# Kernel optimization log

Measured on AMD Instinct MI355X. Metric: run time of the kernel, lower is better.

## Reference

```python
import jax, jax.numpy as jnp
import numpy as np

B, C, K, D = 16, 128, 128, 256
EPS = 1e-5  # torch BatchNorm1d default eps


def _bn(x, gamma, beta):
    # torch BatchNorm1d training-mode on (N, ch, L): normalize each channel over (N, L)
    mean = x.mean(axis=(0, 2), keepdims=True)
    var = x.var(axis=(0, 2), keepdims=True)  # biased, matches torch normalization
    return (x - mean) / jnp.sqrt(var + EPS) * gamma[None, :, None] + beta[None, :, None]


def setup_inputs() -> dict:
    key = jax.random.key(0)
    ks = jax.random.split(key, 6)
    q = jax.random.normal(ks[0], (B, C, D), jnp.float32)
    kc = jax.random.normal(ks[1], (B, K, D), jnp.float32)
    W0 = jax.random.normal(ks[2], (D, D), jnp.float32) / np.sqrt(D)
    W1 = jax.random.normal(ks[3], (D, D), jnp.float32) / np.sqrt(D)
    cmask = jax.random.randint(ks[4], (B, C), 0, 2, jnp.int32)
    kmask = jax.random.randint(ks[5], (B, K), 0, 2, jnp.int32)
    klen = jnp.maximum(kmask.sum(axis=1), 1).astype(jnp.int32)
    return {
        "query_candidates_repr": q,
        "key_candidates": kc,
        "W0": W0,
        "W1": W1,
        "bn0_gamma": jnp.ones((C,), jnp.float32),
        "bn0_beta": jnp.zeros((C,), jnp.float32),
        "bn1_gamma": jnp.ones((K,), jnp.float32),
        "bn1_beta": jnp.zeros((K,), jnp.float32),
        "query_candidate_mask": cmask,
        "key_candidate_mask": kmask,
        "key_candidate_len": klen,
    }


def reference(query_candidates_repr, key_candidates, W0, W1,
              bn0_gamma, bn0_beta, bn1_gamma, bn1_beta,
              query_candidate_mask, key_candidate_mask, key_candidate_len):
    # gated_attention branch (att_type != 'softmax'), activate = tanh
    g0 = _bn(query_candidates_repr @ W0.T, bn0_gamma, bn0_beta)  # (B,C,D)
    g1 = _bn(key_candidates @ W1.T, bn1_gamma, bn1_beta)          # (B,K,D)
    # (B,C,K,D) gate product
    attention_weight = jax.nn.sigmoid(g1)[:, None, :, :] * jax.nn.sigmoid(g0)[:, :, None, :]
    attention_res = key_candidates[:, None, :, :] * attention_weight  # (B,C,K,D)
    mask = (query_candidate_mask[:, :, None] * key_candidate_mask[:, None, :]).astype(jnp.float32)
    attention_res_masked = attention_res * mask[..., None]
    attention_vector = attention_res_masked.sum(axis=2) / key_candidate_len[:, None, None].astype(jnp.float32)
    output_res = jnp.tanh(attention_vector)  # (B,C,D)
    return output_res, attention_res_masked, attention_weight.mean(axis=-1)
```

## Files before the change

kernel.cpp:

```cpp
#include <hip/hip_runtime.h>


#define NB 16
#define NC 128
#define NK 128
#define ND 256

__global__ __launch_bounds__(256) void k_gemm(const float* __restrict__ q,
                                              const float* __restrict__ kc,
                                              const float* __restrict__ W0,
                                              const float* __restrict__ W1,
                                              float* __restrict__ Y,
                                              float* __restrict__ tvec) {
    if (blockIdx.x == 0 && blockIdx.y == 0) {
        for (int i = threadIdx.x; i < NB * ND; i += 256) tvec[i] = 0.f;
    }
    __shared__ float As[16][64];
    __shared__ float Bs[16][64];
    const int m0 = blockIdx.x * 64;
    const int d0 = blockIdx.y * 64;
    const int t  = threadIdx.x;
    const float* A = (m0 < 2048) ? (q + (size_t)m0 * ND) : (kc + (size_t)(m0 - 2048) * ND);
    const float* W = (m0 < 2048) ? W0 : W1;
    const int ml = t >> 2;
    const int jl = (t & 3) * 4;
    const int ty = t >> 4;
    const int tx = t & 15;

    float acc[4][4] = {};
    for (int j0 = 0; j0 < 256; j0 += 16) {
        float4 a = *(const float4*)(A + ml * ND + j0 + jl);
        float4 b = *(const float4*)(W + (d0 + ml) * ND + j0 + jl);
        As[jl + 0][ml] = a.x; As[jl + 1][ml] = a.y; As[jl + 2][ml] = a.z; As[jl + 3][ml] = a.w;
        Bs[jl + 0][ml] = b.x; Bs[jl + 1][ml] = b.y; Bs[jl + 2][ml] = b.z; Bs[jl + 3][ml] = b.w;
        __syncthreads();
#pragma unroll
        for (int jj = 0; jj < 16; ++jj) {
            float4 av = *(const float4*)&As[jj][ty * 4];
            float4 bv = *(const float4*)&Bs[jj][tx * 4];
            acc[0][0] += av.x * bv.x; acc[0][1] += av.x * bv.y; acc[0][2] += av.x * bv.z; acc[0][3] += av.x * bv.w;
            acc[1][0] += av.y * bv.x; acc[1][1] += av.y * bv.y; acc[1][2] += av.y * bv.z; acc[1][3] += av.y * bv.w;
            acc[2][0] += av.z * bv.x; acc[2][1] += av.z * bv.y; acc[2][2] += av.z * bv.z; acc[2][3] += av.z * bv.w;
            acc[3][0] += av.w * bv.x; acc[3][1] += av.w * bv.y; acc[3][2] += av.w * bv.z; acc[3][3] += av.w * bv.w;
        }
        __syncthreads();
    }
#pragma unroll
    for (int i = 0; i < 4; ++i) {
        float4 o = make_float4(acc[i][0], acc[i][1], acc[i][2], acc[i][3]);
        *(float4*)(Y + (size_t)(m0 + ty * 4 + i) * ND + d0 + tx * 4) = o;
    }
}

__global__ __launch_bounds__(256) void k_sau(float* __restrict__ Y,
                                             const float* __restrict__ kc,
                                             const float* __restrict__ g0, const float* __restrict__ b0,
                                             const float* __restrict__ g1, const float* __restrict__ b1,
                                             const int* __restrict__ kmask,
                                             float* __restrict__ tvec) {
    const int ch = blockIdx.x;
    const int t  = threadIdx.x;
    const int rbase = (ch < 128) ? ch : (2048 + (ch - 128));
    float v[NB];
    float s = 0.f, s2 = 0.f;
#pragma unroll
    for (int b = 0; b < NB; ++b) {
        v[b] = Y[(size_t)(rbase + b * 128) * ND + t];
        s += v[b]; s2 += v[b] * v[b];
    }
#pragma unroll
    for (int off = 32; off > 0; off >>= 1) {
        s  += __shfl_down(s,  off, 64);
        s2 += __shfl_down(s2, off, 64);
    }
    __shared__ float r1[4], r2[4];
    __shared__ float bsc, bsh;
    const int w = t >> 6;
    if ((t & 63) == 0) { r1[w] = s; r2[w] = s2; }
    __syncthreads();
    if (t == 0) {
        s  = r1[0] + r1[1] + r1[2] + r1[3];
        s2 = r2[0] + r2[1] + r2[2] + r2[3];
        float mean = s * (1.f / 4096.f);
        float var  = s2 * (1.f / 4096.f) - mean * mean;
        float rstd = rsqrtf(var + 1e-5f);
        float g  = (ch < 128) ? g0[ch] : g1[ch - 128];
        float be = (ch < 128) ? b0[ch] : b1[ch - 128];
        bsc = g * rstd;
        bsh = be - mean * g * rstd;
    }
    __syncthreads();
    const float sc = bsc, sh = bsh;
    if (ch < 128) {
#pragma unroll
        for (int b = 0; b < NB; ++b) {
            float sig = 1.f / (1.f + __expf(-(v[b] * sc + sh)));
            Y[(size_t)(rbase + b * 128) * ND + t] = sig;
        }
    } else {
        const int k = ch - 128;
#pragma unroll
        for (int b = 0; b < NB; ++b) {
            float sig = 1.f / (1.f + __expf(-(v[b] * sc + sh)));
            Y[(size_t)(rbase + b * 128) * ND + t] = sig;
            if (kmask[b * 128 + k] != 0) {
                float u = kc[(size_t)(b * 128 + k) * ND + t] * sig;
                atomicAdd(&tvec[b * ND + t], u);
            }
        }
    }
}

__global__ __launch_bounds__(256) void k_tail(const float* __restrict__ Y,
                                              const float* __restrict__ kc,
                                              const int* __restrict__ cmask,
                                              const int* __restrict__ kmask,
                                              const int* __restrict__ klen,
                                              const float* __restrict__ tvec,
                                              float* __restrict__ out0,
                                              float* __restrict__ out1,
                                              float* __restrict__ out2) {
    __shared__ float As[16][64];
    __shared__ float Bs[16][64];
    const int bid = blockIdx.x;
    const int t   = threadIdx.x;

    if (bid < 64) {
        const int b  = bid >> 2;
        const int c0 = ((bid >> 1) & 1) * 64;
        const int k0 = (bid & 1) * 64;
        const float* A = Y + (size_t)(b * 128 + c0) * ND;
        const float* W = Y + (size_t)(2048 + b * 128 + k0) * ND;
        const int ml = t >> 2;
        const int jl = (t & 3) * 4;
        const int ty = t >> 4;
        const int tx = t & 15;
        float acc[4][4] = {};
        for (int j0 = 0; j0 < 256; j0 += 16) {
            float4 a  = *(const float4*)(A + ml * ND + j0 + jl);
            float4 bb = *(const float4*)(W + ml * ND + j0 + jl);
            As[jl + 0][ml] = a.x;  As[jl + 1][ml] = a.y;  As[jl + 2][ml] = a.z;  As[jl + 3][ml] = a.w;
            Bs[jl + 0][ml] = bb.x; Bs[jl + 1][ml] = bb.y; Bs[jl + 2][ml] = bb.z; Bs[jl + 3][ml] = bb.w;
            __syncthreads();
#pragma unroll
            for (int jj = 0; jj < 16; ++jj) {
                float4 av = *(const float4*)&As[jj][ty * 4];
                float4 bv = *(const float4*)&Bs[jj][tx * 4];
                acc[0][0] += av.x * bv.x; acc[0][1] += av.x * bv.y; acc[0][2] += av.x * bv.z; acc[0][3] += av.x * bv.w;
                acc[1][0] += av.y * bv.x; acc[1][1] += av.y * bv.y; acc[1][2] += av.y * bv.z; acc[1][3] += av.y * bv.w;
                acc[2][0] += av.z * bv.x; acc[2][1] += av.z * bv.y; acc[2][2] += av.z * bv.z; acc[2][3] += av.z * bv.w;
                acc[3][0] += av.w * bv.x; acc[3][1] += av.w * bv.y; acc[3][2] += av.w * bv.z; acc[3][3] += av.w * bv.w;
            }
            __syncthreads();
        }
        const float scale = 1.f / 256.f;
#pragma unroll
        for (int i = 0; i < 4; ++i) {
            float4 o = make_float4(acc[i][0] * scale, acc[i][1] * scale, acc[i][2] * scale, acc[i][3] * scale);
            *(float4*)(out2 + ((size_t)(b * 128 + c0 + ty * 4 + i)) * 128 + k0 + tx * 4) = o;
        }
    } else if (bid < 320) {
        const int local = bid - 64;
        const int b  = local >> 4;
        const int c0 = (local & 15) * 8;
        const float tv  = tvec[b * ND + t];
        const float inv = 1.f / (float)klen[b];
#pragma unroll
        for (int ci = 0; ci < 8; ++ci) {
            const int bc = b * 128 + c0 + ci;
            const float cm = (cmask[bc] != 0) ? 1.f : 0.f;
            const float s0 = Y[(size_t)bc * ND + t];
            out0[(size_t)bc * ND + t] = tanhf(cm * s0 * tv * inv);
        }
    } else {
        const int bc = bid - 320;
        const int b  = bc >> 7;
        const int f  = t & 63;
        const int g  = t >> 6;
        float4 s0v = *(const float4*)(Y + (size_t)bc * ND + f * 4);
        const bool cm = cmask[bc] != 0;
        float4 v0 = cm ? s0v : make_float4(0.f, 0.f, 0.f, 0.f);

        const float* s1p = Y  + (size_t)(2048 + b * 128 + g) * ND + f * 4;
        const float* kcp = kc + (size_t)(b * 128 + g) * ND + f * 4;
        const int*   kmb = kmask + b * 128;
        float*       op  = out1 + (size_t)bc * 128 * ND + (size_t)g * ND + f * 4;

#pragma unroll 4
        for (int k0 = 0; k0 < 32; ++k0) {
            const int k = k0 * 4 + g;
            const float km = (float)kmb[k];
            float4 s1v = *(const float4*)s1p;
            float4 kcv = *(const float4*)kcp;
            float4 o = make_float4(v0.x * km * kcv.x * s1v.x,
                                   v0.y * km * kcv.y * s1v.y,
                                   v0.z * km * kcv.z * s1v.z,
                                   v0.w * km * kcv.w * s1v.w);
            *(float4*)op = o;
            s1p += 4 * ND; kcp += 4 * ND; op += 4 * ND;
        }
    }
}

extern "C" void kernel_launch(void* const* d_in, const int* in_sizes, int n_in,
                              void* d_out, int out_size, void* d_ws, size_t ws_size,
                              hipStream_t stream) {
    const float* q     = (const float*)d_in[0];
    const float* kc    = (const float*)d_in[1];
    const float* W0    = (const float*)d_in[2];
    const float* W1    = (const float*)d_in[3];
    const float* g0    = (const float*)d_in[4];
    const float* b0    = (const float*)d_in[5];
    const float* g1    = (const float*)d_in[6];
    const float* b1    = (const float*)d_in[7];
    const int*   cmask = (const int*)d_in[8];
    const int*   kmask = (const int*)d_in[9];
    const int*   klen  = (const int*)d_in[10];

    float* ws = (float*)d_ws;
    float* Y  = ws;
    float* tv = ws + 1048576;

    float* o    = (float*)d_out;
    float* out0 = o;
    float* out1 = o + 524288;
    float* out2 = o + 67633152;

    k_gemm<<<dim3(64, 4), 256, 0, stream>>>(q, kc, W0, W1, Y, tv);
    k_sau <<<256,         256, 0, stream>>>(Y, kc, g0, b0, g1, b1, kmask, tv);
    k_tail<<<2368,        256, 0, stream>>>(Y, kc, cmask, kmask, klen, tv, out0, out1, out2);
}
```

Measured before the change: 324.4 us.

## Precompute masked key*gate product, remap blocks per XCD, use nontemporal stores

k_sau now writes a precomputed per-key product U = kmask*kc*sigmoid(g1) into the workspace. The big out1 write loop therefore reads one stream instead of two plus the mask. The block-to-(b,c) mapping is permuted so that consecutive block ids, which are spread across XCDs, share the same batch's U rows in each XCD's L2. Output stores for the 256MB out1 tensor become nontemporal to avoid polluting cache. This adds an extra 2MB write in k_sau in exchange.

```diff
diff --git a/kernel.cpp b/kernel.cpp
--- a/kernel.cpp
+++ b/kernel.cpp
@@ -5,6 +5,8 @@
 #define NC 128
 #define NK 128
 #define ND 256
+
+typedef float f4v __attribute__((ext_vector_type(4)));
 
 __global__ __launch_bounds__(256) void k_gemm(const float* __restrict__ q,
                                               const float* __restrict__ kc,
@@ -57,6 +59,7 @@
                                              const float* __restrict__ g0, const float* __restrict__ b0,
                                              const float* __restrict__ g1, const float* __restrict__ b1,
                                              const int* __restrict__ kmask,
+                                             float* __restrict__ U,
                                              float* __restrict__ tvec) {
     const int ch = blockIdx.x;
     const int t  = threadIdx.x;
@@ -103,18 +106,21 @@
         for (int b = 0; b < NB; ++b) {
             float sig = 1.f / (1.f + __expf(-(v[b] * sc + sh)));
             Y[(size_t)(rbase + b * 128) * ND + t] = sig;
-            if (kmask[b * 128 + k] != 0) {
-                float u = kc[(size_t)(b * 128 + k) * ND + t] * sig;
+            const int r = b * 128 + k;
+            if (kmask[r] != 0) {
+                float u = kc[(size_t)r * ND + t] * sig;
+                U[(size_t)r * ND + t] = u;
                 atomicAdd(&tvec[b * ND + t], u);
+            } else {
+                U[(size_t)r * ND + t] = 0.f;
             }
         }
     }
 }
 
 __global__ __launch_bounds__(256) void k_tail(const float* __restrict__ Y,
-                                              const float* __restrict__ kc,
+                                              const float* __restrict__ U,
                                               const int* __restrict__ cmask,
-                                              const int* __restrict__ kmask,
                                               const int* __restrict__ klen,
                                               const float* __restrict__ tvec,
                                               float* __restrict__ out0,
@@ -173,32 +179,32 @@
             out0[(size_t)bc * ND + t] = tanhf(cm * s0 * tv * inv);
         }
     } else {
-        const int bc = bid - 320;
-        const int b  = bc >> 7;
-        const int f  = t & 63;
-        const int g  = t >> 6;
+        const int s   = bid - 320;
+        const int xcd = s & 7;
+        const int j   = s >> 3;
+        const int b   = (xcd << 1) | (j >> 7);
+        const int c   = j & 127;
+        const int bc  = b * 128 + c;
+        const int f   = t & 63;
+        const int g   = t >> 6;
+
         float4 s0v = *(const float4*)(Y + (size_t)bc * ND + f * 4);
         const bool cm = cmask[bc] != 0;
         float4 v0 = cm ? s0v : make_float4(0.f, 0.f, 0.f, 0.f);
 
-        const float* s1p = Y  + (size_t)(2048 + b * 128 + g) * ND + f * 4;
-        const float* kcp = kc + (size_t)(b * 128 + g) * ND + f * 4;
-        const int*   kmb = kmask + b * 128;
-        float*       op  = out1 + (size_t)bc * 128 * ND + (size_t)g * ND + f * 4;
-
-#pragma unroll 4
+        const float* up = U    + (size_t)(b * 128 + g) * ND + f * 4;
+        float*       op = out1 + (size_t)bc * 128 * ND + (size_t)g * ND + f * 4;
+
+#pragma unroll 8
         for (int k0 = 0; k0 < 32; ++k0) {
-            const int k = k0 * 4 + g;
-            const float km = (float)kmb[k];
-            float4 s1v = *(const float4*)s1p;
-            float4 kcv = *(const float4*)kcp;
-            float4 o = make_float4(v0.x * km * kcv.x * s1v.x,
-                                   v0.y * km * kcv.y * s1v.y,
-                                   v0.z * km * kcv.z * s1v.z,
-                                   v0.w * km * kcv.w * s1v.w);
-            *(float4*)op = o;
-            s1p += 4 * ND; kcp += 4 * ND; op += 4 * ND;
-        }
+            float4 uv = *(const float4*)up;
+            float4 o = make_float4(v0.x * uv.x, v0.y * uv.y, v0.z * uv.z, v0.w * uv.w);
+            __builtin_nontemporal_store(*(const f4v*)&o, (f4v*)op);
+            up += 4 * ND;
+            op += 4 * ND;
+        }
+
+        if (g == 0 && false) {  }
     }
 }
 
@@ -220,6 +226,7 @@
     float* ws = (float*)d_ws;
     float* Y  = ws;
     float* tv = ws + 1048576;
+    float* U  = ws + 1052672;
 
     float* o    = (float*)d_out;
     float* out0 = o;
@@ -227,6 +234,6 @@
     float* out2 = o + 67633152;
 
     k_gemm<<<dim3(64, 4), 256, 0, stream>>>(q, kc, W0, W1, Y, tv);
-    k_sau <<<256,         256, 0, stream>>>(Y, kc, g0, b0, g1, b1, kmask, tv);
-    k_tail<<<2368,        256, 0, stream>>>(Y, kc, cmask, kmask, klen, tv, out0, out1, out2);
-}
+    k_sau <<<256,         256, 0, stream>>>(Y, kc, g0, b0, g1, b1, kmask, U, tv);
+    k_tail<<<2368,        256, 0, stream>>>(Y, U, cmask, klen, tv, out0, out1, out2);
+}
```

Measured after the change: 320.1 us. No clear change (-1.3%).
